# Performance work log

Hardware: AMD Instinct MI355X
Metric: run time of the kernel (lower is better)

Reference implementation:

```python
import jax, jax.numpy as jnp
import numpy as np

B = 4        # pair batch
V = 2        # num_views
C = 256      # channels
NH = 4       # num_heads
H = 128
W = 128
G = 8        # GroupNorm groups
EPS = 1e-5


def setup_inputs() -> dict:
    key = jax.random.key(0)
    ks = jax.random.split(key, 5)
    x = jax.random.normal(ks[0], (B * V, C, H, W), jnp.float32)
    gn_gamma = jnp.ones((C,), jnp.float32)
    gn_beta = jnp.zeros((C,), jnp.float32)
    w_qkv = jax.random.normal(ks[1], (3 * C, C), jnp.float32) * 0.02
    b_qkv = jax.random.normal(ks[2], (3 * C,), jnp.float32) * 0.02
    w_proj = jax.random.normal(ks[3], (C, C), jnp.float32) * 0.02
    b_proj = jax.random.normal(ks[4], (C,), jnp.float32) * 0.02
    return {"x": x, "gn_gamma": gn_gamma, "gn_beta": gn_beta,
            "w_qkv": w_qkv, "b_qkv": b_qkv, "w_proj": w_proj, "b_proj": b_proj}


def reference(x, gn_gamma, gn_beta, w_qkv, b_qkv, w_proj, b_proj):
    bv, c, h, w = x.shape
    v, nh = V, NH
    hd = c // nh
    b = bv // v
    scale = hd ** -0.5

    # GroupNorm(8, c): normalize over (c/G, h, w) per group, biased variance
    xg = x.reshape(bv, G, c // G, h, w)
    mean = xg.mean(axis=(2, 3, 4), keepdims=True)
    var = xg.var(axis=(2, 3, 4), keepdims=True)
    xn = ((xg - mean) * jax.lax.rsqrt(var + EPS)).reshape(bv, c, h, w)
    xn = xn * gn_gamma[:, None, None] + gn_beta[:, None, None]

    # 1x1 conv qkv: (bv, 3c, h, w)
    qkv = jnp.einsum('oc,bchw->bohw', w_qkv, xn) + b_qkv[:, None, None]

    # '(b v) (three nh hd) h w -> three b nh (h w) v hd'
    qkv = qkv.reshape(b, v, 3, nh, hd, h * w).transpose(2, 0, 3, 5, 1, 4)
    q, k, val = qkv[0], qkv[1], qkv[2]  # each (b, nh, hw, v, hd)

    # tiny VxV attention per pixel
    attn = jax.nn.softmax(jnp.einsum('bnpvd,bnpud->bnpvu', q, k) * scale, axis=-1)
    out = jnp.einsum('bnpvu,bnpud->bnpvd', attn, val)  # (b, nh, hw, v, hd)

    # 'b nh (h w) v hd -> (b v) (nh hd) h w'
    out = out.transpose(0, 3, 1, 4, 2).reshape(bv, c, h, w)

    # proj 1x1 conv + residual
    out = jnp.einsum('oc,bchw->bohw', w_proj, out) + b_proj[:, None, None]
    return x + out
```

## Files before the change

kernel.cpp:

```cpp
#include <hip/hip_runtime.h>
#include <stdint.h>

#define HW 16384
#define CCH 256
#define NROWS 131072
#define GROUP_ELEMS 524288
#define BK 64
#define LDSP 72

typedef __attribute__((ext_vector_type(8))) short bfrag8;
typedef __attribute__((ext_vector_type(8))) unsigned short us8;
typedef __attribute__((ext_vector_type(4))) float facc4;

static __device__ __forceinline__ unsigned short f2b(float f) {
  union { float f; unsigned int u; } x; x.f = f;
  unsigned int r = x.u + 0x7FFFu + ((x.u >> 16) & 1u);
  return (unsigned short)(r >> 16);
}
static __device__ __forceinline__ float b2f(unsigned short h) {
  union { float f; unsigned int u; } x; x.u = ((unsigned int)h) << 16;
  return x.f;
}

__global__ void k_red(const float* __restrict__ x, float* __restrict__ red) {
  int gg = blockIdx.x >> 3, sp = blockIdx.x & 7;
  const float4* p = (const float4*)(x + (size_t)gg * GROUP_ELEMS + (size_t)sp * 65536);
  float s = 0.f, ss = 0.f;
  for (int i = 0; i < 64; ++i) {
    float4 v = p[i * 256 + threadIdx.x];
    s  += v.x + v.y + v.z + v.w;
    ss += v.x*v.x + v.y*v.y + v.z*v.z + v.w*v.w;
  }
  for (int off = 32; off; off >>= 1) { s += __shfl_xor(s, off); ss += __shfl_xor(ss, off); }
  __shared__ float ls[4], lss[4];
  int w = threadIdx.x >> 6;
  if ((threadIdx.x & 63) == 0) { ls[w] = s; lss[w] = ss; }
  __syncthreads();
  if (threadIdx.x == 0) {
    float S = ls[0]+ls[1]+ls[2]+ls[3], SS = lss[0]+lss[1]+lss[2]+lss[3];
    atomicAdd(&red[gg*2], S); atomicAdd(&red[gg*2+1], SS);
  }
}

__global__ void k_fin(const float* __restrict__ red, float* __restrict__ stats) {
  int g = threadIdx.x;
  float s = red[g*2], ss = red[g*2+1];
  float mean = s / (float)GROUP_ELEMS;
  float var = ss / (float)GROUP_ELEMS - mean*mean;
  stats[g*2] = mean;
  stats[g*2+1] = rsqrtf(var + 1e-5f);
}

__global__ void k_cast(const float* __restrict__ wq, const float* __restrict__ wp,
                       unsigned short* __restrict__ wqb, unsigned short* __restrict__ wpb) {
  int i = blockIdx.x * 256 + threadIdx.x;
  if (i < 768*256) {
    int op = i >> 8, k = i & 255;
    int h = op / 192, cl = op % 192;
    int part = cl >> 6, d = cl & 63;
    int o = part*256 + h*64 + d;
    wqb[i] = f2b(wq[o*256 + k]);
  } else {
    int j = i - 768*256;
    wpb[j] = f2b(wp[j]);
  }
}

__global__ void k_norm_t(const float* __restrict__ x, const float* __restrict__ stats,
                         const float* __restrict__ gamma, const float* __restrict__ beta,
                         unsigned short* __restrict__ xnt) {
  __shared__ float tile[64][65];
  int bx = blockIdx.x;
  int bv = bx >> 10;
  int rem = bx & 1023;
  int p0 = (rem >> 2) * 64, c0 = (rem & 3) * 64;
  int pair = bv >> 1, v = bv & 1;
  int t = threadIdx.x;
  int p_off = t & 63, c4 = t >> 6;
  const float* xsrc = x + (size_t)bv * CCH * HW;
  for (int cc = 0; cc < 16; ++cc) {
    int c_loc = c4 * 16 + cc;
    int c = c0 + c_loc;
    float val = xsrc[(size_t)c * HW + p0 + p_off];
    int g = bv * 8 + (c >> 5);
    float xn = (val - stats[g*2]) * stats[g*2+1] * gamma[c] + beta[c];
    tile[p_off][c_loc] = xn;
  }
  __syncthreads();
  for (int it = 0; it < 8; ++it) {
    int u = it * 256 + t;
    int p = u >> 5, c2 = u & 31;
    unsigned int pk = (unsigned int)f2b(tile[p][c2*2]) | ((unsigned int)f2b(tile[p][c2*2+1]) << 16);
    size_t row = (size_t)pair * 32768 + (size_t)(p0 + p) * 2 + v;
    *(unsigned int*)(xnt + row * 256 + c0 + c2*2) = pk;
  }
}

__global__ __launch_bounds__(256, 2) void k_qkv_attn(
    const unsigned short* __restrict__ A,
    const unsigned short* __restrict__ B,
    const float* __restrict__ bq,
    unsigned short* __restrict__ attn_out) {
  __shared__ __align__(16) unsigned short smem[320 * LDSP];
  unsigned short* As = smem;
  unsigned short* Bs = smem + 128 * LDSP;
  int h = blockIdx.x;
  int row0 = blockIdx.y * 128;
  int t = threadIdx.x;
  int w = t >> 6, lane = t & 63;
  int lm = lane & 15, q4 = lane >> 4;
  const unsigned short* Bh = B + (size_t)h * 192 * 256;

  facc4 acc[2][12];
  #pragma unroll
  for (int j = 0; j < 12; ++j) {
    facc4 bb = *(const facc4*)(bq + (j >> 2)*256 + h*64 + (j & 3)*16 + q4*4);
    acc[0][j] = bb; acc[1][j] = bb;
  }

  for (int kc = 0; kc < 4; ++kc) {
    #pragma unroll
    for (int i = 0; i < 4; ++i) {
      int flat = i * 256 + t;
      int r = flat >> 3, g = flat & 7;
      *(us8*)(&As[r*LDSP + g*8]) = *(const us8*)(A + (size_t)(row0 + r)*256 + kc*BK + g*8);
    }
    #pragma unroll
    for (int i = 0; i < 6; ++i) {
      int flat = i * 256 + t;
      int r = flat >> 3, g = flat & 7;
      *(us8*)(&Bs[r*LDSP + g*8]) = *(const us8*)(Bh + (size_t)r*256 + kc*BK + g*8);
    }
    __syncthreads();
    #pragma unroll
    for (int ks = 0; ks < 2; ++ks) {
      bfrag8 a0 = *(const bfrag8*)(&As[(w*32 +      lm)*LDSP + ks*32 + q4*8]);
      bfrag8 a1 = *(const bfrag8*)(&As[(w*32 + 16 + lm)*LDSP + ks*32 + q4*8]);
      #pragma unroll
      for (int j = 0; j < 12; ++j) {
        bfrag8 wf = *(const bfrag8*)(&Bs[(j*16 + lm)*LDSP + ks*32 + q4*8]);
        acc[0][j] = __builtin_amdgcn_mfma_f32_16x16x32_bf16(wf, a0, acc[0][j], 0, 0, 0);
        acc[1][j] = __builtin_amdgcn_mfma_f32_16x16x32_bf16(wf, a1, acc[1][j], 0, 0, 0);
      }
    }
    __syncthreads();
  }

  #pragma unroll
  for (int i = 0; i < 2; ++i) {
    float s_same = 0.f, s_cross = 0.f;
    #pragma unroll
    for (int jj = 0; jj < 4; ++jj) {
      #pragma unroll
      for (int r = 0; r < 4; ++r) {
        float qv = acc[i][jj][r];
        float kv = acc[i][4 + jj][r];
        float kx = __shfl_xor(kv, 1);
        s_same  += qv * kv;
        s_cross += qv * kx;
      }
    }
    s_same  += __shfl_xor(s_same, 16);  s_same  += __shfl_xor(s_same, 32);
    s_cross += __shfl_xor(s_cross, 16); s_cross += __shfl_xor(s_cross, 32);
    float s0 = s_same * 0.125f, s1 = s_cross * 0.125f;
    float m = fmaxf(s0, s1);
    float e0 = __expf(s0 - m), e1 = __expf(s1 - m);
    float inv = 1.f / (e0 + e1);
    float w_self = e0 * inv, w_cross = e1 * inv;

    int rglob = row0 + w*32 + i*16 + lm;
    int pair = rglob >> 15, rem = rglob & 32767;
    int p = rem >> 1, v = rem & 1;
    unsigned short* dst = attn_out + ((size_t)((pair*2 + v)*16384 + p))*256 + h*64 + q4*4;
    #pragma unroll
    for (int jj = 0; jj < 4; ++jj) {
      float o[4];
      #pragma unroll
      for (int r = 0; r < 4; ++r) {
        float vv = acc[i][8 + jj][r];
        float vx = __shfl_xor(vv, 1);
        o[r] = w_self * vv + w_cross * vx;
      }
      uint2 pk;
      pk.x = (unsigned int)f2b(o[0]) | ((unsigned int)f2b(o[1]) << 16);
      pk.y = (unsigned int)f2b(o[2]) | ((unsigned int)f2b(o[3]) << 16);
      *(uint2*)(dst + jj*16) = pk;
    }
  }
}

__global__ __launch_bounds__(256, 2) void k_gemm_proj(
    const unsigned short* __restrict__ A,
    const unsigned short* __restrict__ B,
    const float* __restrict__ bias,
    const float* __restrict__ x,
    float* __restrict__ out) {
  __shared__ unsigned short As[128][LDSP];
  __shared__ unsigned short Bs[128][LDSP];
  int col0 = blockIdx.x * 128;
  int row0 = blockIdx.y * 128;
  int t = threadIdx.x;
  int w = t >> 6, lane = t & 63;
  int wm = w & 1, wn = w >> 1;
  int lm = lane & 15, q = lane >> 4;
  facc4 acc[4][4] = {};
  for (int kc = 0; kc < 4; ++kc) {
    for (int i = 0; i < 4; ++i) {
      int flat = i * 256 + t;
      int r = flat >> 3, g = flat & 7;
      *(us8*)(&As[r][g*8]) = *(const us8*)(A + (size_t)(row0 + r)*256 + kc*BK + g*8);
      *(us8*)(&Bs[r][g*8]) = *(const us8*)(B + (size_t)(col0 + r)*256 + kc*BK + g*8);
    }
    __syncthreads();
    for (int ks = 0; ks < 2; ++ks) {
      bfrag8 a[4], b[4];
      for (int i = 0; i < 4; ++i) a[i] = *(const bfrag8*)(&As[wm*64 + i*16 + lm][ks*32 + q*8]);
      for (int j = 0; j < 4; ++j) b[j] = *(const bfrag8*)(&Bs[wn*64 + j*16 + lm][ks*32 + q*8]);
      for (int i = 0; i < 4; ++i)
        for (int j = 0; j < 4; ++j)
          acc[i][j] = __builtin_amdgcn_mfma_f32_16x16x32_bf16(a[i], b[j], acc[i][j], 0, 0, 0);
    }
    __syncthreads();
  }
  for (int i = 0; i < 4; ++i) {
    for (int r = 0; r < 4; ++r) {
      int o = row0 + wm*64 + i*16 + q*4 + r;
      float bi = bias[o];
      for (int j = 0; j < 4; ++j) {
        int n = col0 + wn*64 + j*16 + lm;
        int bv = n >> 14, p = n & 16383;
        size_t gidx = ((size_t)bv * 256 + o) * 16384 + p;
        out[gidx] = acc[i][j][r] + bi + x[gidx];
      }
    }
  }
}

extern "C" void kernel_launch(void* const* d_in, const int* in_sizes, int n_in,
                              void* d_out, int out_size, void* d_ws, size_t ws_size,
                              hipStream_t stream) {
  const float* x     = (const float*)d_in[0];
  const float* gamma = (const float*)d_in[1];
  const float* beta  = (const float*)d_in[2];
  const float* wq    = (const float*)d_in[3];
  const float* bq    = (const float*)d_in[4];
  const float* wp    = (const float*)d_in[5];
  const float* bp    = (const float*)d_in[6];
  float* out = (float*)d_out;

  char* ws = (char*)d_ws;
  float* red   = (float*)ws;
  float* stats = (float*)(ws + 512);
  unsigned short* wqb = (unsigned short*)(ws + 1024);
  unsigned short* wpb = (unsigned short*)(ws + 1024 + 393216);
  size_t off = 1024 + 393216 + 131072;
  unsigned short* xnt = (unsigned short*)(ws + off); off += (size_t)NROWS * 256 * 2;
  unsigned short* att = (unsigned short*)(ws + off);

  hipMemsetAsync(red, 0, 1024, stream);
  k_cast<<<1024, 256, 0, stream>>>(wq, wp, wqb, wpb);
  k_red<<<512, 256, 0, stream>>>(x, red);
  k_fin<<<1, 64, 0, stream>>>(red, stats);
  k_norm_t<<<8192, 256, 0, stream>>>(x, stats, gamma, beta, xnt);
  k_qkv_attn<<<dim3(4, 1024), 256, 0, stream>>>(xnt, wqb, bq, att);
  k_gemm_proj<<<dim3(1024, 2), 256, 0, stream>>>(wpb, att, bp, x, out);
}
```

Measured before the change: 462.1 us.

## Pre-swizzle activations and weights into MFMA fragment layout, drop LDS staging

The normalize-transpose kernel and the weight cast kernel now write their bf16 outputs directly in the per-lane MFMA fragment order, with the two views of a pixel placed 8 rows apart. The fused QKV+attention kernel then loads fragments straight from global memory with contiguous 16-byte per-lane reads, which removes the shared-memory staging and the block barriers. The view-pairing shuffle changes from xor 1 to xor 8 to match the new row order. The trade-off is that the weight fragments, shared by all row-blocks, are now re-read from global/L2 by every wave, with no LDS reuse and less latency hiding.

```diff
diff --git a/kernel.cpp b/kernel.cpp
--- a/kernel.cpp
+++ b/kernel.cpp
@@ -55,10 +55,18 @@
                        unsigned short* __restrict__ wqb, unsigned short* __restrict__ wpb) {
   int i = blockIdx.x * 256 + threadIdx.x;
   if (i < 768*256) {
-    int op = i >> 8, k = i & 255;
-    int h = op / 192, cl = op % 192;
+    int h = i / 49152;
+    int rem = i % 49152;
+    int kk = rem / 6144;
+    int rem2 = rem % 6144;
+    int j = rem2 >> 9;
+    int lane = (rem2 >> 3) & 63;
+    int e = rem2 & 7;
+    int q4 = lane >> 4, lm = lane & 15;
+    int cl = j*16 + lm;
     int part = cl >> 6, d = cl & 63;
     int o = part*256 + h*64 + d;
+    int k = kk*32 + q4*8 + e;
     wqb[i] = f2b(wq[o*256 + k]);
   } else {
     int j = i - 768*256;
@@ -90,9 +98,14 @@
   for (int it = 0; it < 8; ++it) {
     int u = it * 256 + t;
     int p = u >> 5, c2 = u & 31;
+    int c = c0 + c2*2;
     unsigned int pk = (unsigned int)f2b(tile[p][c2*2]) | ((unsigned int)f2b(tile[p][c2*2+1]) << 16);
-    size_t row = (size_t)pair * 32768 + (size_t)(p0 + p) * 2 + v;
-    *(unsigned int*)(xnt + row * 256 + c0 + c2*2) = pk;
+    int P = p0 + p;
+    int n = pair*2048 + (P >> 3);
+    int s = (P & 7) + 8*v;
+    size_t addr = (size_t)n*4096 + (size_t)(c >> 5)*512 + (size_t)((c & 31) >> 3)*128
+                + (size_t)s*8 + (c & 7);
+    *(unsigned int*)(xnt + addr) = pk;
   }
 }
 
@@ -101,15 +114,14 @@
     const unsigned short* __restrict__ B,
     const float* __restrict__ bq,
     unsigned short* __restrict__ attn_out) {
-  __shared__ __align__(16) unsigned short smem[320 * LDSP];
-  unsigned short* As = smem;
-  unsigned short* Bs = smem + 128 * LDSP;
   int h = blockIdx.x;
   int row0 = blockIdx.y * 128;
   int t = threadIdx.x;
   int w = t >> 6, lane = t & 63;
   int lm = lane & 15, q4 = lane >> 4;
-  const unsigned short* Bh = B + (size_t)h * 192 * 256;
+
+  size_t aBase = (size_t)((row0 + w*32) >> 4) * 4096 + (size_t)lane * 8;
+  size_t bBase = (size_t)h * 49152 + (size_t)lane * 8;
 
   facc4 acc[2][12];
   #pragma unroll
@@ -118,32 +130,16 @@
     acc[0][j] = bb; acc[1][j] = bb;
   }
 
-  for (int kc = 0; kc < 4; ++kc) {
+  #pragma unroll
+  for (int kk = 0; kk < 8; ++kk) {
+    bfrag8 a0 = *(const bfrag8*)(A + aBase + (size_t)kk*512);
+    bfrag8 a1 = *(const bfrag8*)(A + aBase + 4096 + (size_t)kk*512);
     #pragma unroll
-    for (int i = 0; i < 4; ++i) {
-      int flat = i * 256 + t;
-      int r = flat >> 3, g = flat & 7;
-      *(us8*)(&As[r*LDSP + g*8]) = *(const us8*)(A + (size_t)(row0 + r)*256 + kc*BK + g*8);
-    }
-    #pragma unroll
-    for (int i = 0; i < 6; ++i) {
-      int flat = i * 256 + t;
-      int r = flat >> 3, g = flat & 7;
-      *(us8*)(&Bs[r*LDSP + g*8]) = *(const us8*)(Bh + (size_t)r*256 + kc*BK + g*8);
-    }
-    __syncthreads();
-    #pragma unroll
-    for (int ks = 0; ks < 2; ++ks) {
-      bfrag8 a0 = *(const bfrag8*)(&As[(w*32 +      lm)*LDSP + ks*32 + q4*8]);
-      bfrag8 a1 = *(const bfrag8*)(&As[(w*32 + 16 + lm)*LDSP + ks*32 + q4*8]);
-      #pragma unroll
-      for (int j = 0; j < 12; ++j) {
-        bfrag8 wf = *(const bfrag8*)(&Bs[(j*16 + lm)*LDSP + ks*32 + q4*8]);
-        acc[0][j] = __builtin_amdgcn_mfma_f32_16x16x32_bf16(wf, a0, acc[0][j], 0, 0, 0);
-        acc[1][j] = __builtin_amdgcn_mfma_f32_16x16x32_bf16(wf, a1, acc[1][j], 0, 0, 0);
-      }
-    }
-    __syncthreads();
+    for (int j = 0; j < 12; ++j) {
+      bfrag8 wf = *(const bfrag8*)(B + bBase + (size_t)(kk*12 + j)*512);
+      acc[0][j] = __builtin_amdgcn_mfma_f32_16x16x32_bf16(wf, a0, acc[0][j], 0, 0, 0);
+      acc[1][j] = __builtin_amdgcn_mfma_f32_16x16x32_bf16(wf, a1, acc[1][j], 0, 0, 0);
+    }
   }
 
   #pragma unroll
@@ -155,7 +151,7 @@
       for (int r = 0; r < 4; ++r) {
         float qv = acc[i][jj][r];
         float kv = acc[i][4 + jj][r];
-        float kx = __shfl_xor(kv, 1);
+        float kx = __shfl_xor(kv, 8);
         s_same  += qv * kv;
         s_cross += qv * kx;
       }
@@ -168,9 +164,10 @@
     float inv = 1.f / (e0 + e1);
     float w_self = e0 * inv, w_cross = e1 * inv;
 
-    int rglob = row0 + w*32 + i*16 + lm;
-    int pair = rglob >> 15, rem = rglob & 32767;
-    int p = rem >> 1, v = rem & 1;
+    int rg = row0 + w*32 + i*16;
+    int pg = (rg >> 1) + (lm & 7);
+    int v = lm >> 3;
+    int pair = pg >> 14, p = pg & 16383;
     unsigned short* dst = attn_out + ((size_t)((pair*2 + v)*16384 + p))*256 + h*64 + q4*4;
     #pragma unroll
     for (int jj = 0; jj < 4; ++jj) {
@@ -178,7 +175,7 @@
       #pragma unroll
       for (int r = 0; r < 4; ++r) {
         float vv = acc[i][8 + jj][r];
-        float vx = __shfl_xor(vv, 1);
+        float vx = __shfl_xor(vv, 8);
         o[r] = w_self * vv + w_cross * vx;
       }
       uint2 pk;
```

Measured after the change: 477.3 us. 3.3% more time.
